# Optimization experiments

Hardware: AMD Instinct MI355X
Metric: run time of the kernel (lower is better)

## Reference

```python
import jax, jax.numpy as jnp
import numpy as np


def setup_inputs() -> dict:
    key = jax.random.key(0)
    k1, k2, k3 = jax.random.split(key, 3)
    B, D, H, W, K = 16, 512, 60, 60, 32
    std = 1.0 / np.sqrt(K * D)
    X = jax.random.normal(k1, (B, D, H, W), dtype=jnp.float32)
    codewords = jax.random.uniform(k2, (K, D), dtype=jnp.float32, minval=-std, maxval=std)
    # scale is drawn uniform(-1, 0) in the torch module (shake in train mode)
    scale = -jax.random.uniform(k3, (K,), dtype=jnp.float32)
    return {"X": X, "codewords": codewords, "scale": scale}


def reference(X, codewords, scale):
    # X: (B, D, H, W) -> flatten spatial to (B, N, D)
    B, D = X.shape[0], X.shape[1]
    Xf = X.reshape(B, D, -1).transpose(0, 2, 1)          # (B, N, D)
    # scaledL2: SL[b,n,k] = scale[k] * ||X[b,n] - C[k]||^2, expanded via GEMM
    # to avoid the (B, N, K, D) residual tensor.
    x2 = jnp.sum(Xf * Xf, axis=-1)                       # (B, N)
    c2 = jnp.sum(codewords * codewords, axis=-1)         # (K,)
    xc = jnp.einsum('bnd,kd->bnk', Xf, codewords)        # (B, N, K)
    sl = scale * (x2[..., None] - 2.0 * xc + c2)         # (B, N, K)
    A = jax.nn.softmax(sl, axis=2)                       # (B, N, K)
    # aggregate: E[b,k,d] = sum_n A[b,n,k] * (X[b,n,d] - C[k,d])
    E = jnp.einsum('bnk,bnd->bkd', A, Xf) - jnp.sum(A, axis=1)[..., None] * codewords
    return E                                             # (B, K, D)
```

## Files before the change

kernel.cpp:

```cpp
#include <hip/hip_runtime.h>
#include <hip/hip_bf16.h>

constexpr int BB = 16;
constexpr int DD = 512;
constexpr int NN = 3600;
constexpr int KK = 32;
constexpr int SB = 29;
constexpr int WIN = 128;

typedef __attribute__((ext_vector_type(8))) short short8;
typedef __attribute__((ext_vector_type(4))) float f32x4;

__device__ inline unsigned bf16pack(float a, float b) {
    unsigned ia = __float_as_uint(a), ib = __float_as_uint(b);
    ia = (ia + 0x7fffu + ((ia >> 16) & 1u)) >> 16;
    ib = (ib + 0x7fffu + ((ib >> 16) & 1u)) & 0xffff0000u;
    return ia | ib;
}

__global__ __launch_bounds__(256) void k0_prep(const float* __restrict__ Cw,
                                               const float* __restrict__ scale,
                                               ushort* __restrict__ Cbf,
                                               float* __restrict__ sc2) {
    __shared__ float buf[8][32];
    const int t = threadIdx.x;
    const int k = t & 31;
    const int h = t >> 5;
    const float4* row = reinterpret_cast<const float4*>(Cw + k * DD + h * 64);
    uint2* crow = reinterpret_cast<uint2*>(Cbf + k * DD + h * 64);
    float s = 0.f;
#pragma unroll
    for (int j = 0; j < 16; ++j) {
        float4 v = row[j];
        crow[j] = make_uint2(bf16pack(v.x, v.y), bf16pack(v.z, v.w));
        s += v.x * v.x + v.y * v.y + v.z * v.z + v.w * v.w;
    }
    buf[h][k] = s;
    __syncthreads();
    if (t < 32) {
        float tot = 0.f;
#pragma unroll
        for (int j = 0; j < 8; ++j) tot += buf[j][t];
        sc2[t] = scale[t] * tot;
    }
}

__global__ __launch_bounds__(512, 2) void kf_fused(const float* __restrict__ X,
                                                   const ushort* __restrict__ Cbf,
                                                   const float* __restrict__ scale,
                                                   const float* __restrict__ sc2,
                                                   float* __restrict__ Ep,
                                                   float* __restrict__ asum_part) {
    __shared__ ushort tile[DD * WIN];
    __shared__ ushort As2[KK * WIN];
    __shared__ float x2part[16][WIN];
    __shared__ float x2s[WIN];
    __shared__ float asw[8][KK];

    const int t = threadIdx.x;
    const int w = t >> 6;
    const int l = t & 63;
    const int q = l >> 4;
    const int r = l & 15;
    const int ng = t & 31;
    const int dgs = t >> 5;
    const int b = blockIdx.x / SB;
    const int sb = blockIdx.x % SB;
    const int n0 = sb * WIN;
    const float* Xb = X + (size_t)b * DD * NN;
    const ushort* cb0 = Cbf + r * DD + q * 8;
    const ushort* cb1 = cb0 + 16 * DD;

    int nst = n0 + ng * 4;
    if (nst > NN - 4) nst = NN - 4;
    const float* xsrc = Xb + nst;

    const int nloc = w * 16 + r;
    f32x4 a0 = {0.f, 0.f, 0.f, 0.f};
    f32x4 a1 = {0.f, 0.f, 0.f, 0.f};
    float x2loc[4] = {0.f, 0.f, 0.f, 0.f};

    float4 bufA[8], bufB[8];
#pragma unroll
    for (int i = 0; i < 8; ++i)
        bufA[i] = *reinterpret_cast<const float4*>(xsrc + (size_t)(dgs * 8 + i) * NN);

#define CHUNK_BODY(CURB, NXTB, C)                                              \
    {                                                                          \
        short8 cf0[4], cf1[4];                                                 \
        _Pragma("unroll")                                                      \
        for (int u = 0; u < 4; ++u) {                                          \
            cf0[u] = *reinterpret_cast<const short8*>(cb0 + ((C)*4 + u) * 32); \
            cf1[u] = *reinterpret_cast<const short8*>(cb1 + ((C)*4 + u) * 32); \
        }                                                                      \
        if ((C) < 3) {                                                         \
            _Pragma("unroll")                                                  \
            for (int i = 0; i < 8; ++i)                                        \
                NXTB[i] = *reinterpret_cast<const float4*>(                    \
                    xsrc + (size_t)(((C) + 1) * 128 + dgs * 8 + i) * NN);      \
        }                                                                      \
        _Pragma("unroll")                                                      \
        for (int i = 0; i < 8; ++i) {                                          \
            const float4 v = CURB[i];                                          \
            x2loc[0] = fmaf(v.x, v.x, x2loc[0]);                               \
            x2loc[1] = fmaf(v.y, v.y, x2loc[1]);                               \
            x2loc[2] = fmaf(v.z, v.z, x2loc[2]);                               \
            x2loc[3] = fmaf(v.w, v.w, x2loc[3]);                               \
            const int d = (C) * 128 + dgs * 8 + i;                             \
            *reinterpret_cast<uint2*>(                                         \
                &tile[d * WIN + ((ng * 4) ^ ((d & 7) << 3))]) =                \
                make_uint2(bf16pack(v.x, v.y), bf16pack(v.z, v.w));            \
        }                                                                      \
        asm volatile("s_waitcnt lgkmcnt(0)" ::: "memory");                     \
        __builtin_amdgcn_s_barrier();                                          \
        __builtin_amdgcn_sched_barrier(0);                                     \
        _Pragma("unroll")                                                      \
        for (int u = 0; u < 4; ++u) {                                          \
            const int s = (C) * 4 + u;                                         \
            union { short8 s8; ushort us[8]; } af;                             \
            _Pragma("unroll")                                                  \
            for (int jj = 0; jj < 8; ++jj)                                     \
                af.us[jj] = tile[(s * 32 + q * 8 + jj) * WIN + (nloc ^ (jj << 3))]; \
            a0 = __builtin_amdgcn_mfma_f32_16x16x32_bf16(af.s8, cf0[u], a0, 0, 0, 0); \
            a1 = __builtin_amdgcn_mfma_f32_16x16x32_bf16(af.s8, cf1[u], a1, 0, 0, 0); \
        }                                                                      \
    }

    CHUNK_BODY(bufA, bufB, 0)
    CHUNK_BODY(bufB, bufA, 1)
    CHUNK_BODY(bufA, bufB, 2)
    CHUNK_BODY(bufB, bufA, 3)
#undef CHUNK_BODY

    *reinterpret_cast<f32x4*>(&x2part[dgs][ng * 4]) =
        (f32x4){x2loc[0], x2loc[1], x2loc[2], x2loc[3]};
    __syncthreads();
    if (t < WIN) {
        float s = 0.f;
#pragma unroll
        for (int dg = 0; dg < 16; ++dg) s += x2part[dg][t];
        x2s[t] = s;
    }
    __syncthreads();

    const float sk0 = scale[r], sk1 = scale[r + 16];
    const float sq0 = sc2[r],  sq1 = sc2[r + 16];
    float e0v[4], e1v[4];
    float as0 = 0.f, as1 = 0.f;
#pragma unroll
    for (int i = 0; i < 4; ++i) {
        const float x2v = x2s[w * 16 + 4 * q + i];
        float sl0 = fmaf(sk0, x2v, sq0) - 2.f * sk0 * a0[i];
        float sl1 = fmaf(sk1, x2v, sq1) - 2.f * sk1 * a1[i];
        float m = fmaxf(sl0, sl1);
        m = fmaxf(m, __shfl_xor(m, 1));
        m = fmaxf(m, __shfl_xor(m, 2));
        m = fmaxf(m, __shfl_xor(m, 4));
        m = fmaxf(m, __shfl_xor(m, 8));
        float e0 = __expf(sl0 - m), e1 = __expf(sl1 - m);
        float ssum = e0 + e1;
        ssum += __shfl_xor(ssum, 1);
        ssum += __shfl_xor(ssum, 2);
        ssum += __shfl_xor(ssum, 4);
        ssum += __shfl_xor(ssum, 8);
        const float inv = 1.f / ssum;
        e0 *= inv; e1 *= inv;
        if (n0 + w * 16 + 4 * q + i >= NN) { e0 = 0.f; e1 = 0.f; }
        e0v[i] = e0; e1v[i] = e1;
        as0 += e0; as1 += e1;
    }
    *reinterpret_cast<uint2*>(&As2[r * WIN + ((w * 16 + 4 * q) ^ ((r & 7) << 3))]) =
        make_uint2(bf16pack(e0v[0], e0v[1]), bf16pack(e0v[2], e0v[3]));
    *reinterpret_cast<uint2*>(&As2[(r + 16) * WIN + ((w * 16 + 4 * q) ^ ((r & 7) << 3))]) =
        make_uint2(bf16pack(e1v[0], e1v[1]), bf16pack(e1v[2], e1v[3]));

    as0 += __shfl_xor(as0, 16); as0 += __shfl_xor(as0, 32);
    as1 += __shfl_xor(as1, 16); as1 += __shfl_xor(as1, 32);
    if (l < 16) { asw[w][r] = as0; asw[w][r + 16] = as1; }
    __syncthreads();
    if (t < KK) {
        float s = 0.f;
#pragma unroll
        for (int jw = 0; jw < 8; ++jw) s += asw[jw][t];
        asum_part[((size_t)b * SB + sb) * KK + t] = s;
    }

    short8 bfr0[4], bfr1[4];
#pragma unroll
    for (int step = 0; step < 4; ++step) {
        bfr0[step] = *reinterpret_cast<const short8*>(
            &As2[r * WIN + ((step * 32 + q * 8) ^ ((r & 7) << 3))]);
        bfr1[step] = *reinterpret_cast<const short8*>(
            &As2[(r + 16) * WIN + ((step * 32 + q * 8) ^ ((r & 7) << 3))]);
    }

    f32x4 acc[4][2];
#pragma unroll
    for (int df = 0; df < 4; ++df) {
        acc[df][0] = (f32x4){0.f, 0.f, 0.f, 0.f};
        acc[df][1] = (f32x4){0.f, 0.f, 0.f, 0.f};
    }

#pragma unroll
    for (int df = 0; df < 4; ++df) {
        const int d = w * 64 + df * 16 + r;
#pragma unroll
        for (int step = 0; step < 4; ++step) {
            const short8 xa = *reinterpret_cast<const short8*>(
                &tile[d * WIN + ((step * 32 + q * 8) ^ ((d & 7) << 3))]);
            acc[df][0] = __builtin_amdgcn_mfma_f32_16x16x32_bf16(
                xa, bfr0[step], acc[df][0], 0, 0, 0);
            acc[df][1] = __builtin_amdgcn_mfma_f32_16x16x32_bf16(
                xa, bfr1[step], acc[df][1], 0, 0, 0);
        }
    }

    float* ep = Ep + (size_t)(b * SB + sb) * KK * DD;
#pragma unroll
    for (int df = 0; df < 4; ++df) {
#pragma unroll
        for (int kf = 0; kf < 2; ++kf) {
            const int k = kf * 16 + r;
            const int d = w * 64 + df * 16 + q * 4;
            *reinterpret_cast<f32x4*>(ep + (size_t)k * DD + d) = acc[df][kf];
        }
    }
}

__global__ __launch_bounds__(256) void k3_final(const float* __restrict__ Ep,
                                                const float* __restrict__ asum_part,
                                                const float* __restrict__ Cw,
                                                float* __restrict__ E) {
    const int t = threadIdx.x;
    const int b = blockIdx.x >> 5, k = blockIdx.x & 31;

    float asum = 0.f;
#pragma unroll
    for (int sb = 0; sb < SB; ++sb)
        asum += asum_part[((size_t)b * SB + sb) * KK + k];

#pragma unroll
    for (int h = 0; h < 2; ++h) {
        const int d = t + h * 256;
        float s2 = 0.f;
#pragma unroll 4
        for (int sb = 0; sb < SB; ++sb)
            s2 += Ep[(((size_t)b * SB + sb) * KK + k) * DD + d];
        E[((size_t)b * KK + k) * DD + d] = s2 - asum * Cw[k * DD + d];
    }
}

extern "C" void kernel_launch(void* const* d_in, const int* in_sizes, int n_in,
                              void* d_out, int out_size, void* d_ws, size_t ws_size,
                              hipStream_t stream) {
    const float* X     = (const float*)d_in[0];
    const float* Cw    = (const float*)d_in[1];
    const float* scale = (const float*)d_in[2];
    float* E = (float*)d_out;

    float* ws = (float*)d_ws;
    float* Ep = ws;
    float* asum_part = Ep + (size_t)BB * SB * KK * DD;
    float* sc2 = asum_part + (size_t)BB * SB * KK;
    ushort* Cbf = (ushort*)(sc2 + KK);

    k0_prep<<<dim3(1), dim3(256), 0, stream>>>(Cw, scale, Cbf, sc2);
    kf_fused<<<dim3(BB * SB), dim3(512), 0, stream>>>(X, Cbf, scale, sc2, Ep, asum_part);
    k3_final<<<dim3(BB * KK), dim3(256), 0, stream>>>(Ep, asum_part, Cw, E);
}
```

Before: 57.95 us.

## Halve spatial window, shrink blocks, store bf16 partials, swizzle LDS by row group

```diff
diff --git a/kernel.cpp b/kernel.cpp
--- a/kernel.cpp
+++ b/kernel.cpp
@@ -5,8 +5,8 @@
 constexpr int DD = 512;
 constexpr int NN = 3600;
 constexpr int KK = 32;
-constexpr int SB = 29;
-constexpr int WIN = 128;
+constexpr int SBW = 57;
+constexpr int WIN = 64;
 
 typedef __attribute__((ext_vector_type(8))) short short8;
 typedef __attribute__((ext_vector_type(4))) float f32x4;
@@ -16,6 +16,10 @@
     ia = (ia + 0x7fffu + ((ia >> 16) & 1u)) >> 16;
     ib = (ib + 0x7fffu + ((ib >> 16) & 1u)) & 0xffff0000u;
     return ia | ib;
+}
+
+__device__ inline int swzkey(int row) {
+    return ((row ^ (row >> 3)) & 7) << 3;
 }
 
 __global__ __launch_bounds__(256) void k0_prep(const float* __restrict__ Cw,
@@ -45,27 +49,27 @@
     }
 }
 
-__global__ __launch_bounds__(512, 2) void kf_fused(const float* __restrict__ X,
+__global__ __launch_bounds__(256, 2) void kf_fused(const float* __restrict__ X,
                                                    const ushort* __restrict__ Cbf,
                                                    const float* __restrict__ scale,
                                                    const float* __restrict__ sc2,
-                                                   float* __restrict__ Ep,
+                                                   ushort* __restrict__ Epb,
                                                    float* __restrict__ asum_part) {
     __shared__ ushort tile[DD * WIN];
     __shared__ ushort As2[KK * WIN];
     __shared__ float x2part[16][WIN];
     __shared__ float x2s[WIN];
-    __shared__ float asw[8][KK];
+    __shared__ float asw[4][KK];
 
     const int t = threadIdx.x;
     const int w = t >> 6;
     const int l = t & 63;
     const int q = l >> 4;
     const int r = l & 15;
-    const int ng = t & 31;
-    const int dgs = t >> 5;
-    const int b = blockIdx.x / SB;
-    const int sb = blockIdx.x % SB;
+    const int ng = t & 15;
+    const int dd = t >> 4;
+    const int b = blockIdx.x / SBW;
+    const int sb = blockIdx.x % SBW;
     const int n0 = sb * WIN;
     const float* Xb = X + (size_t)b * DD * NN;
     const ushort* cb0 = Cbf + r * DD + q * 8;
@@ -83,7 +87,7 @@
     float4 bufA[8], bufB[8];
 #pragma unroll
     for (int i = 0; i < 8; ++i)
-        bufA[i] = *reinterpret_cast<const float4*>(xsrc + (size_t)(dgs * 8 + i) * NN);
+        bufA[i] = *reinterpret_cast<const float4*>(xsrc + (size_t)(dd * 8 + i) * NN);
 
 #define CHUNK_BODY(CURB, NXTB, C)                                              \
     {                                                                          \
@@ -97,7 +101,7 @@
             _Pragma("unroll")                                                  \
             for (int i = 0; i < 8; ++i)                                        \
                 NXTB[i] = *reinterpret_cast<const float4*>(                    \
-                    xsrc + (size_t)(((C) + 1) * 128 + dgs * 8 + i) * NN);      \
+                    xsrc + (size_t)(((C) + 1) * 128 + dd * 8 + i) * NN);       \
         }                                                                      \
         _Pragma("unroll")                                                      \
         for (int i = 0; i < 8; ++i) {                                          \
@@ -106,9 +110,9 @@
             x2loc[1] = fmaf(v.y, v.y, x2loc[1]);                               \
             x2loc[2] = fmaf(v.z, v.z, x2loc[2]);                               \
             x2loc[3] = fmaf(v.w, v.w, x2loc[3]);                               \
-            const int d = (C) * 128 + dgs * 8 + i;                             \
+            const int d = (C) * 128 + dd * 8 + i;                              \
             *reinterpret_cast<uint2*>(                                         \
-                &tile[d * WIN + ((ng * 4) ^ ((d & 7) << 3))]) =                \
+                &tile[d * WIN + ((ng * 4) ^ swzkey(d))]) =                     \
                 make_uint2(bf16pack(v.x, v.y), bf16pack(v.z, v.w));            \
         }                                                                      \
         asm volatile("s_waitcnt lgkmcnt(0)" ::: "memory");                     \
@@ -119,8 +123,10 @@
             const int s = (C) * 4 + u;                                         \
             union { short8 s8; ushort us[8]; } af;                             \
             _Pragma("unroll")                                                  \
-            for (int jj = 0; jj < 8; ++jj)                                     \
-                af.us[jj] = tile[(s * 32 + q * 8 + jj) * WIN + (nloc ^ (jj << 3))]; \
+            for (int jj = 0; jj < 8; ++jj) {                                   \
+                const int dA = s * 32 + q * 8 + jj;                            \
+                af.us[jj] = tile[dA * WIN + (nloc ^ swzkey(dA))];              \
+            }                                                                  \
             a0 = __builtin_amdgcn_mfma_f32_16x16x32_bf16(af.s8, cf0[u], a0, 0, 0, 0); \
             a1 = __builtin_amdgcn_mfma_f32_16x16x32_bf16(af.s8, cf1[u], a1, 0, 0, 0); \
         }                                                                      \
@@ -132,7 +138,7 @@
     CHUNK_BODY(bufB, bufA, 3)
 #undef CHUNK_BODY
 
-    *reinterpret_cast<f32x4*>(&x2part[dgs][ng * 4]) =
+    *reinterpret_cast<f32x4*>(&x2part[dd][ng * 4]) =
         (f32x4){x2loc[0], x2loc[1], x2loc[2], x2loc[3]};
     __syncthreads();
     if (t < WIN) {
@@ -169,9 +175,9 @@
         e0v[i] = e0; e1v[i] = e1;
         as0 += e0; as1 += e1;
     }
-    *reinterpret_cast<uint2*>(&As2[r * WIN + ((w * 16 + 4 * q) ^ ((r & 7) << 3))]) =
+    *reinterpret_cast<uint2*>(&As2[r * WIN + ((w * 16 + 4 * q) ^ swzkey(r))]) =
         make_uint2(bf16pack(e0v[0], e0v[1]), bf16pack(e0v[2], e0v[3]));
-    *reinterpret_cast<uint2*>(&As2[(r + 16) * WIN + ((w * 16 + 4 * q) ^ ((r & 7) << 3))]) =
+    *reinterpret_cast<uint2*>(&As2[(r + 16) * WIN + ((w * 16 + 4 * q) ^ swzkey(r + 16))]) =
         make_uint2(bf16pack(e1v[0], e1v[1]), bf16pack(e1v[2], e1v[3]));
 
     as0 += __shfl_xor(as0, 16); as0 += __shfl_xor(as0, 32);
@@ -181,33 +187,34 @@
     if (t < KK) {
         float s = 0.f;
 #pragma unroll
-        for (int jw = 0; jw < 8; ++jw) s += asw[jw][t];
-        asum_part[((size_t)b * SB + sb) * KK + t] = s;
-    }
-
-    short8 bfr0[4], bfr1[4];
-#pragma unroll
-    for (int step = 0; step < 4; ++step) {
+        for (int jw = 0; jw < 4; ++jw) s += asw[jw][t];
+        asum_part[((size_t)b * SBW + sb) * KK + t] = s;
+    }
+
+    short8 bfr0[2], bfr1[2];
+#pragma unroll
+    for (int step = 0; step < 2; ++step) {
         bfr0[step] = *reinterpret_cast<const short8*>(
-            &As2[r * WIN + ((step * 32 + q * 8) ^ ((r & 7) << 3))]);
+            &As2[r * WIN + ((step * 32 + q * 8) ^ swzkey(r))]);
         bfr1[step] = *reinterpret_cast<const short8*>(
-            &As2[(r + 16) * WIN + ((step * 32 + q * 8) ^ ((r & 7) << 3))]);
-    }
-
-    f32x4 acc[4][2];
-#pragma unroll
-    for (int df = 0; df < 4; ++df) {
+            &As2[(r + 16) * WIN + ((step * 32 + q * 8) ^ swzkey(r + 16))]);
+    }
+
+    f32x4 acc[8][2];
+#pragma unroll
+    for (int df = 0; df < 8; ++df) {
         acc[df][0] = (f32x4){0.f, 0.f, 0.f, 0.f};
         acc[df][1] = (f32x4){0.f, 0.f, 0.f, 0.f};
     }
 
 #pragma unroll
-    for (int df = 0; df < 4; ++df) {
-        const int d = w * 64 + df * 16 + r;
-#pragma unroll
-        for (int step = 0; step < 4; ++step) {
+    for (int df = 0; df < 8; ++df) {
+        const int d = w * 128 + df * 16 + r;
+        const int kd = swzkey(d);
+#pragma unroll
+        for (int step = 0; step < 2; ++step) {
             const short8 xa = *reinterpret_cast<const short8*>(
-                &tile[d * WIN + ((step * 32 + q * 8) ^ ((d & 7) << 3))]);
+                &tile[d * WIN + ((step * 32 + q * 8) ^ kd)]);
             acc[df][0] = __builtin_amdgcn_mfma_f32_16x16x32_bf16(
                 xa, bfr0[step], acc[df][0], 0, 0, 0);
             acc[df][1] = __builtin_amdgcn_mfma_f32_16x16x32_bf16(
@@ -215,19 +222,21 @@
         }
     }
 
-    float* ep = Ep + (size_t)(b * SB + sb) * KK * DD;
-#pragma unroll
-    for (int df = 0; df < 4; ++df) {
+    ushort* ep = Epb + (size_t)(b * SBW + sb) * KK * DD;
+#pragma unroll
+    for (int df = 0; df < 8; ++df) {
 #pragma unroll
         for (int kf = 0; kf < 2; ++kf) {
             const int k = kf * 16 + r;
-            const int d = w * 64 + df * 16 + q * 4;
-            *reinterpret_cast<f32x4*>(ep + (size_t)k * DD + d) = acc[df][kf];
+            const int d = w * 128 + df * 16 + q * 4;
+            const f32x4 v = acc[df][kf];
+            *reinterpret_cast<uint2*>(ep + (size_t)k * DD + d) =
+                make_uint2(bf16pack(v[0], v[1]), bf16pack(v[2], v[3]));
         }
     }
 }
 
-__global__ __launch_bounds__(256) void k3_final(const float* __restrict__ Ep,
+__global__ __launch_bounds__(256) void k3_final(const ushort* __restrict__ Epb,
                                                 const float* __restrict__ asum_part,
                                                 const float* __restrict__ Cw,
                                                 float* __restrict__ E) {
@@ -236,18 +245,23 @@
 
     float asum = 0.f;
 #pragma unroll
-    for (int sb = 0; sb < SB; ++sb)
-        asum += asum_part[((size_t)b * SB + sb) * KK + k];
-
-#pragma unroll
-    for (int h = 0; h < 2; ++h) {
-        const int d = t + h * 256;
-        float s2 = 0.f;
+    for (int sb = 0; sb < SBW; ++sb)
+        asum += asum_part[((size_t)b * SBW + sb) * KK + k];
+
+    const int d = t * 2;
+    float s0 = 0.f, s1 = 0.f;
 #pragma unroll 4
-        for (int sb = 0; sb < SB; ++sb)
-            s2 += Ep[(((size_t)b * SB + sb) * KK + k) * DD + d];
-        E[((size_t)b * KK + k) * DD + d] = s2 - asum * Cw[k * DD + d];
-    }
+    for (int sb = 0; sb < SBW; ++sb) {
+        const unsigned u = *reinterpret_cast<const unsigned*>(
+            Epb + (((size_t)b * SBW + sb) * KK + k) * DD + d);
+        s0 += __uint_as_float(u << 16);
+        s1 += __uint_as_float(u & 0xffff0000u);
+    }
+    float2 c = *reinterpret_cast<const float2*>(Cw + k * DD + d);
+    float2 o;
+    o.x = s0 - asum * c.x;
+    o.y = s1 - asum * c.y;
+    *reinterpret_cast<float2*>(E + ((size_t)b * KK + k) * DD + d) = o;
 }
 
 extern "C" void kernel_launch(void* const* d_in, const int* in_sizes, int n_in,
@@ -259,12 +273,12 @@
     float* E = (float*)d_out;
 
     float* ws = (float*)d_ws;
-    float* Ep = ws;
-    float* asum_part = Ep + (size_t)BB * SB * KK * DD;
-    float* sc2 = asum_part + (size_t)BB * SB * KK;
+    ushort* Epb = (ushort*)ws;
+    float* asum_part = ws + (size_t)BB * SBW * KK * DD / 2;
+    float* sc2 = asum_part + (size_t)BB * SBW * KK;
     ushort* Cbf = (ushort*)(sc2 + KK);
 
     k0_prep<<<dim3(1), dim3(256), 0, stream>>>(Cw, scale, Cbf, sc2);
-    kf_fused<<<dim3(BB * SB), dim3(512), 0, stream>>>(X, Cbf, scale, sc2, Ep, asum_part);
-    k3_final<<<dim3(BB * KK), dim3(256), 0, stream>>>(Ep, asum_part, Cw, E);
-}
+    kf_fused<<<dim3(BB * SBW), dim3(256), 0, stream>>>(X, Cbf, scale, sc2, Epb, asum_part);
+    k3_final<<<dim3(BB * KK), dim3(256), 0, stream>>>(Epb, asum_part, Cw, E);
+}
```

Measured after the change: 62.09 us. 7.1% more time.
